# Performance work log

Measured on AMD Instinct MI355X. Metric: run time of the kernel, lower is better.

## Reference

```python
import jax, jax.numpy as jnp
from jax import lax
import numpy as np

N_RES = 2048
N_IN = 64
N_OUT = 32
T = 4096
SPECTRAL_RADIUS = 0.95
NOISE = 0.001


def setup_inputs() -> dict:
    key = jax.random.key(0)
    ks = jax.random.split(key, 8)
    # recurrent weights: uniform(-0.5, 0.5) rescaled to target spectral radius
    w_raw = np.asarray(jax.random.uniform(ks[0], (N_RES, N_RES))) - 0.5
    radius = np.max(np.abs(np.linalg.eigvals(w_raw)))
    w = jnp.asarray((w_raw * (SPECTRAL_RADIUS / radius)).astype(np.float32))
    w_in = jax.random.uniform(ks[1], (N_RES, N_IN), dtype=jnp.float32) * 2.0 - 1.0
    w_feedb = jax.random.uniform(ks[2], (N_RES, N_OUT), dtype=jnp.float32) * 2.0 - 1.0
    # readout (nn.Linear)
    out_w = jax.random.normal(ks[3], (N_OUT, N_RES), dtype=jnp.float32) * 0.02
    out_b = jax.random.normal(ks[4], (N_OUT,), dtype=jnp.float32) * 0.02
    inputs = jax.random.normal(ks[5], (T, N_IN), dtype=jnp.float32)
    outputs = jax.random.normal(ks[6], (T, N_OUT), dtype=jnp.float32)
    # per-step uniform noise (torch.rand equivalent), precomputed for determinism
    noise_u = jax.random.uniform(ks[7], (T, N_RES), dtype=jnp.float32)
    return {"inputs": inputs, "outputs": outputs, "w": w, "w_in": w_in,
            "w_feedb": w_feedb, "out_w": out_w, "out_b": out_b, "noise_u": noise_u}


def reference(inputs, outputs, w, w_in, w_feedb, out_w, out_b, noise_u):
    # Faithful ESN forward with teacher forcing:
    #   state[n] = tanh(w @ state[n-1] + w_in @ inputs[n] + w_feedb @ outputs[n-1])
    #              + noise * (u[n] - 0.5),   n = 1..T-1, state[0] = 0
    # returns (Linear(state[-1]), state[-1])
    def step(state, xs):
        inp, outp_prev, nu = xs
        pre = w @ state + w_in @ inp + w_feedb @ outp_prev
        new_state = jnp.tanh(pre) + NOISE * (nu - 0.5)
        return new_state, None

    state0 = jnp.zeros((w.shape[0],), dtype=inputs.dtype)
    last_state, _ = lax.scan(step, state0, (inputs[1:], outputs[:-1], noise_u[1:]))
    out_activation = out_w @ last_state + out_b
    return out_activation, last_state
```

## Files before the change

kernel.cpp:

```cpp
#include <hip/hip_runtime.h>


#define N_RES   2048
#define N_IN    64
#define N_OUT   32
#define T_STEPS 4096
#define NOISEC  0.001f
#define NBLK    256
#define NTHR    256
#define RPB     8
#define CPT     8

typedef float f32x4 __attribute__((ext_vector_type(4)));

__device__ __forceinline__ float fast_tanh(float x) {
    const float e = __builtin_amdgcn_exp2f(2.8853900818f * x);
    return fmaf(-2.f, __builtin_amdgcn_rcpf(e + 1.f), 1.f);
}

__global__ void esn_init(unsigned long long* __restrict__ slots) {
    const int i = blockIdx.x * blockDim.x + threadIdx.x;
    if (i < 2 * N_RES)
        __hip_atomic_store(slots + i, 0ull, __ATOMIC_RELAXED, __HIP_MEMORY_SCOPE_AGENT);
}

__global__ __launch_bounds__(NTHR, 1)
void esn_run(const float* __restrict__ inputs,
             const float* __restrict__ outputs,
             const float* __restrict__ w,
             const float* __restrict__ w_in,
             const float* __restrict__ w_feedb,
             const float* __restrict__ out_w,
             const float* __restrict__ out_b,
             const float* __restrict__ noise_u,
             float* __restrict__ d_out,
             unsigned long long* __restrict__ slots) {
    const int tid  = threadIdx.x;
    const int blk  = blockIdx.x;
    const int row0 = blk * RPB;
    const int wav  = tid >> 6;
    const int lan  = tid & 63;

    __shared__ float wlds[2 * 8 * NTHR * 4];
    __shared__ float red[2][4][RPB];

    #pragma unroll
    for (int r = 0; r < RPB; ++r)
        #pragma unroll
        for (int cc = 0; cc < 8; ++cc) {
            const float v = w[(size_t)(row0 + r) * N_RES + cc * NTHR + tid];
            wlds[(((r >> 2) * 8 + cc) * NTHR + tid) * 4 + (r & 3)] = v;
        }
    float wex[RPB];
    #pragma unroll
    for (int r = 0; r < RPB; ++r) {
        float v = 0.f;
        if (tid < N_IN)              v = w_in[(row0 + r) * N_IN + tid];
        else if (tid < N_IN + N_OUT) v = w_feedb[(row0 + r) * N_OUT + (tid - N_IN)];
        wex[r] = v;
    }
    __syncthreads();

    for (int t = 1; t < T_STEPS; ++t) {
        f32x4 wv[16];
        #pragma unroll
        for (int rr = 0; rr < 2; ++rr)
            #pragma unroll
            for (int cc = 0; cc < 8; ++cc)
                wv[rr * 8 + cc] = *reinterpret_cast<const f32x4*>(
                    &wlds[((rr * 8 + cc) * NTHR + tid) * 4]);

        float xv = 0.f;
        if (tid < N_IN)              xv = inputs[t * N_IN + tid];
        else if (tid < N_IN + N_OUT) xv = outputs[(t - 1) * N_OUT + (tid - N_IN)];
        float nu = 0.f;
        if (tid < RPB) nu = noise_u[(size_t)t * N_RES + row0 + tid];

        asm volatile("" ::: "memory");

        const unsigned long long* sl = slots + (size_t)((t - 1) & 1) * N_RES + tid;
        const unsigned need = (unsigned)(t - 1);
        unsigned long long vv[CPT];
        #pragma unroll
        for (int i = 0; i < CPT; ++i)
            vv[i] = __hip_atomic_load(sl + i * NTHR, __ATOMIC_RELAXED, __HIP_MEMORY_SCOPE_AGENT);
        for (;;) {
            unsigned mn = 0xffffffffu;
            #pragma unroll
            for (int i = 0; i < CPT; ++i) {
                const unsigned tg = (unsigned)(vv[i] >> 32);
                mn = (tg < mn) ? tg : mn;
            }
            if (mn >= need) break;
            __builtin_amdgcn_s_sleep(1);
            #pragma unroll
            for (int i = 0; i < CPT; ++i)
                if ((unsigned)(vv[i] >> 32) < need)
                    vv[i] = __hip_atomic_load(sl + i * NTHR, __ATOMIC_RELAXED, __HIP_MEMORY_SCOPE_AGENT);
        }

        float acc[RPB];
        #pragma unroll
        for (int r = 0; r < RPB; ++r) acc[r] = 0.f;
        #pragma unroll
        for (int i = 0; i < CPT; ++i) {
            const float sv = __uint_as_float((unsigned)(vv[i] & 0xffffffffu));
            #pragma unroll
            for (int rr = 0; rr < 2; ++rr)
                #pragma unroll
                for (int j = 0; j < 4; ++j)
                    acc[rr * 4 + j] = fmaf(wv[rr * 8 + i][j], sv, acc[rr * 4 + j]);
        }
        #pragma unroll
        for (int r = 0; r < RPB; ++r) acc[r] = fmaf(wex[r], xv, acc[r]);

        {   const bool b = (lan & 1);
            #pragma unroll
            for (int r = 0; r < 4; ++r) {
                const float send = b ? acc[r] : acc[r + 4];
                const float got  = __shfl_xor(send, 1, 64);
                acc[r] = (b ? acc[r + 4] : acc[r]) + got;
            }
        }
        {   const bool b = (lan >> 1) & 1;
            #pragma unroll
            for (int r = 0; r < 2; ++r) {
                const float send = b ? acc[r] : acc[r + 2];
                const float got  = __shfl_xor(send, 2, 64);
                acc[r] = (b ? acc[r + 2] : acc[r]) + got;
            }
        }
        {   const bool b = (lan >> 2) & 1;
            const float send = b ? acc[0] : acc[1];
            const float got  = __shfl_xor(send, 4, 64);
            acc[0] = (b ? acc[1] : acc[0]) + got;
        }
        #pragma unroll
        for (int m = 8; m < 64; m <<= 1) acc[0] += __shfl_xor(acc[0], m, 64);
        if (lan < 8) {
            const int rb = 4 * (lan & 1) + 2 * ((lan >> 1) & 1) + ((lan >> 2) & 1);
            red[t & 1][wav][rb] = acc[0];
        }
        __syncthreads();

        if (tid < RPB) {
            const float tot = red[t & 1][0][tid] + red[t & 1][1][tid]
                            + red[t & 1][2][tid] + red[t & 1][3][tid];
            const float val = fast_tanh(tot) + NOISEC * (nu - 0.5f);
            const unsigned long long pk =
                ((unsigned long long)(unsigned)t << 32) |
                (unsigned long long)__float_as_uint(val);
            __hip_atomic_store(slots + (size_t)(t & 1) * N_RES + row0 + tid, pk,
                               __ATOMIC_RELAXED, __HIP_MEMORY_SCOPE_AGENT);
            if (t == T_STEPS - 1) d_out[32 + row0 + tid] = val;
        }
    }

    if (blk == 0) {
        const unsigned long long* sf = slots + (size_t)((T_STEPS - 1) & 1) * N_RES;
        const int r2 = tid >> 3, j2 = tid & 7;
        const unsigned need = (unsigned)(T_STEPS - 1);
        float acc = 0.f;
        for (int c0 = 0; c0 < N_RES / 8; c0 += 8) {
            const unsigned long long* p = sf + j2 * (N_RES / 8) + c0;
            unsigned long long vv[8];
            #pragma unroll
            for (int i = 0; i < 8; ++i)
                vv[i] = __hip_atomic_load(p + i, __ATOMIC_RELAXED, __HIP_MEMORY_SCOPE_AGENT);
            for (;;) {
                unsigned mn = 0xffffffffu;
                #pragma unroll
                for (int i = 0; i < 8; ++i) {
                    const unsigned tg = (unsigned)(vv[i] >> 32);
                    mn = (tg < mn) ? tg : mn;
                }
                if (mn >= need) break;
                __builtin_amdgcn_s_sleep(1);
                #pragma unroll
                for (int i = 0; i < 8; ++i)
                    if ((unsigned)(vv[i] >> 32) < need)
                        vv[i] = __hip_atomic_load(p + i, __ATOMIC_RELAXED, __HIP_MEMORY_SCOPE_AGENT);
            }
            #pragma unroll
            for (int i = 0; i < 8; ++i) {
                const float sv = __uint_as_float((unsigned)(vv[i] & 0xffffffffu));
                acc = fmaf(out_w[r2 * N_RES + j2 * (N_RES / 8) + c0 + i], sv, acc);
            }
        }
        #pragma unroll
        for (int m = 1; m < 8; m <<= 1) acc += __shfl_xor(acc, m, 64);
        if (j2 == 0) d_out[r2] = acc + out_b[r2];
    }
}

extern "C" void kernel_launch(void* const* d_in, const int* in_sizes, int n_in,
                              void* d_out, int out_size, void* d_ws, size_t ws_size,
                              hipStream_t stream) {
    const float* inputs  = (const float*)d_in[0];
    const float* outputs = (const float*)d_in[1];
    const float* w       = (const float*)d_in[2];
    const float* w_in    = (const float*)d_in[3];
    const float* w_feedb = (const float*)d_in[4];
    const float* out_w   = (const float*)d_in[5];
    const float* out_b   = (const float*)d_in[6];
    const float* noise_u = (const float*)d_in[7];
    unsigned long long* slots = (unsigned long long*)d_ws;

    esn_init<<<(2 * N_RES + NTHR - 1) / NTHR, NTHR, 0, stream>>>(slots);
    esn_run<<<NBLK, NTHR, 0, stream>>>(inputs, outputs, w, w_in, w_feedb,
                                       out_w, out_b, noise_u,
                                       (float*)d_out, slots);
}
```

Measured before the change: 8.087 ms.

## Halve block count with 16 rows per block and consume state slots incrementally

Each block now owns 16 reservoir rows instead of 8, so 128 blocks replace 256 and fewer producers and consumers take part in the per-step global handshake. The spin-wait now accumulates partial dot products as soon as individual state slots arrive, instead of waiting for all of them first, so polling latency overlaps with FMA work. The slot loads are issued before the LDS weight loads. In exchange, each block carries twice the weight registers and FMA work per step, which raises register pressure and lengthens per-step compute on the critical path.

Result: slower. 10.41 ms (+28.8%).

```diff
diff --git a/kernel.cpp b/kernel.cpp
--- a/kernel.cpp
+++ b/kernel.cpp
@@ -6,9 +6,9 @@
 #define N_OUT   32
 #define T_STEPS 4096
 #define NOISEC  0.001f
-#define NBLK    256
+#define NBLK    128
 #define NTHR    256
-#define RPB     8
+#define RPB     16
 #define CPT     8
 
 typedef float f32x4 __attribute__((ext_vector_type(4)));
@@ -41,7 +41,7 @@
     const int wav  = tid >> 6;
     const int lan  = tid & 63;
 
-    __shared__ float wlds[2 * 8 * NTHR * 4];
+    __shared__ float wlds[4 * 8 * NTHR * 4];
     __shared__ float red[2][4][RPB];
 
     #pragma unroll
@@ -62,13 +62,13 @@
     __syncthreads();
 
     for (int t = 1; t < T_STEPS; ++t) {
-        f32x4 wv[16];
-        #pragma unroll
-        for (int rr = 0; rr < 2; ++rr)
-            #pragma unroll
-            for (int cc = 0; cc < 8; ++cc)
-                wv[rr * 8 + cc] = *reinterpret_cast<const f32x4*>(
-                    &wlds[((rr * 8 + cc) * NTHR + tid) * 4]);
+        const unsigned need = (unsigned)(t - 1);
+        const unsigned long long* sl = slots + (size_t)((t - 1) & 1) * N_RES + tid;
+
+        unsigned long long vv[CPT];
+        #pragma unroll
+        for (int i = 0; i < CPT; ++i)
+            vv[i] = __hip_atomic_load(sl + i * NTHR, __ATOMIC_RELAXED, __HIP_MEMORY_SCOPE_AGENT);
 
         float xv = 0.f;
         if (tid < N_IN)              xv = inputs[t * N_IN + tid];
@@ -76,70 +76,80 @@
         float nu = 0.f;
         if (tid < RPB) nu = noise_u[(size_t)t * N_RES + row0 + tid];
 
+        f32x4 wv[32];
+        #pragma unroll
+        for (int rr = 0; rr < 4; ++rr)
+            #pragma unroll
+            for (int cc = 0; cc < 8; ++cc)
+                wv[rr * 8 + cc] = *reinterpret_cast<const f32x4*>(
+                    &wlds[((rr * 8 + cc) * NTHR + tid) * 4]);
+
         asm volatile("" ::: "memory");
 
-        const unsigned long long* sl = slots + (size_t)((t - 1) & 1) * N_RES + tid;
-        const unsigned need = (unsigned)(t - 1);
-        unsigned long long vv[CPT];
-        #pragma unroll
-        for (int i = 0; i < CPT; ++i)
-            vv[i] = __hip_atomic_load(sl + i * NTHR, __ATOMIC_RELAXED, __HIP_MEMORY_SCOPE_AGENT);
+        float acc[RPB];
+        #pragma unroll
+        for (int r = 0; r < RPB; ++r) acc[r] = 0.f;
+        unsigned done = 0;
         for (;;) {
-            unsigned mn = 0xffffffffu;
-            #pragma unroll
-            for (int i = 0; i < CPT; ++i) {
-                const unsigned tg = (unsigned)(vv[i] >> 32);
-                mn = (tg < mn) ? tg : mn;
-            }
-            if (mn >= need) break;
+            unsigned fresh = 0;
+            #pragma unroll
+            for (int i = 0; i < CPT; ++i)
+                if (!((done >> i) & 1) && (unsigned)(vv[i] >> 32) >= need)
+                    fresh |= 1u << i;
+            #pragma unroll
+            for (int i = 0; i < CPT; ++i)
+                if ((fresh >> i) & 1) {
+                    const float sv = __uint_as_float((unsigned)(vv[i] & 0xffffffffu));
+                    #pragma unroll
+                    for (int rr = 0; rr < 4; ++rr)
+                        #pragma unroll
+                        for (int j = 0; j < 4; ++j)
+                            acc[rr * 4 + j] = fmaf(wv[rr * 8 + i][j], sv, acc[rr * 4 + j]);
+                }
+            done |= fresh;
+            if (done == 0xffu) break;
             __builtin_amdgcn_s_sleep(1);
             #pragma unroll
             for (int i = 0; i < CPT; ++i)
-                if ((unsigned)(vv[i] >> 32) < need)
+                if (!((done >> i) & 1))
                     vv[i] = __hip_atomic_load(sl + i * NTHR, __ATOMIC_RELAXED, __HIP_MEMORY_SCOPE_AGENT);
         }
-
-        float acc[RPB];
-        #pragma unroll
-        for (int r = 0; r < RPB; ++r) acc[r] = 0.f;
-        #pragma unroll
-        for (int i = 0; i < CPT; ++i) {
-            const float sv = __uint_as_float((unsigned)(vv[i] & 0xffffffffu));
-            #pragma unroll
-            for (int rr = 0; rr < 2; ++rr)
-                #pragma unroll
-                for (int j = 0; j < 4; ++j)
-                    acc[rr * 4 + j] = fmaf(wv[rr * 8 + i][j], sv, acc[rr * 4 + j]);
-        }
         #pragma unroll
         for (int r = 0; r < RPB; ++r) acc[r] = fmaf(wex[r], xv, acc[r]);
 
         {   const bool b = (lan & 1);
+            #pragma unroll
+            for (int r = 0; r < 8; ++r) {
+                const float send = b ? acc[r] : acc[r + 8];
+                const float got  = __shfl_xor(send, 1, 64);
+                acc[r] = (b ? acc[r + 8] : acc[r]) + got;
+            }
+        }
+        {   const bool b = (lan >> 1) & 1;
             #pragma unroll
             for (int r = 0; r < 4; ++r) {
                 const float send = b ? acc[r] : acc[r + 4];
-                const float got  = __shfl_xor(send, 1, 64);
+                const float got  = __shfl_xor(send, 2, 64);
                 acc[r] = (b ? acc[r + 4] : acc[r]) + got;
             }
         }
-        {   const bool b = (lan >> 1) & 1;
+        {   const bool b = (lan >> 2) & 1;
             #pragma unroll
             for (int r = 0; r < 2; ++r) {
                 const float send = b ? acc[r] : acc[r + 2];
-                const float got  = __shfl_xor(send, 2, 64);
+                const float got  = __shfl_xor(send, 4, 64);
                 acc[r] = (b ? acc[r + 2] : acc[r]) + got;
             }
         }
-        {   const bool b = (lan >> 2) & 1;
-            const float send = b ? acc[0] : acc[1];
-            const float got  = __shfl_xor(send, 4, 64);
-            acc[0] = (b ? acc[1] : acc[0]) + got;
-        }
-        #pragma unroll
-        for (int m = 8; m < 64; m <<= 1) acc[0] += __shfl_xor(acc[0], m, 64);
+        #pragma unroll
+        for (int m = 8; m < 64; m <<= 1) {
+            acc[0] += __shfl_xor(acc[0], m, 64);
+            acc[1] += __shfl_xor(acc[1], m, 64);
+        }
         if (lan < 8) {
-            const int rb = 4 * (lan & 1) + 2 * ((lan >> 1) & 1) + ((lan >> 2) & 1);
-            red[t & 1][wav][rb] = acc[0];
+            const int rb = 8 * (lan & 1) + 4 * ((lan >> 1) & 1) + 2 * ((lan >> 2) & 1);
+            red[t & 1][wav][rb]     = acc[0];
+            red[t & 1][wav][rb + 1] = acc[1];
         }
         __syncthreads();
 
```

## Use contiguous per-thread state columns and issue slot loads before LDS weight reads

Applied to the files above, without the earlier changes.

Each thread now owns 8 contiguous state columns (tid*8+i), so its polling loads hit adjacent 64-bit slots. Each row of W is re-laid out in LDS to match this mapping. The state slot loads are issued before the LDS weight reads and the x/noise loads, so global latency overlaps them. The spin loop skips the sleep on its first retry and reloads all 8 slots unconditionally instead of only the stale ones. This trades fewer cache lines per thread and lower wake-up latency for more polling traffic and a less coalesced pattern across lanes.

New measurement: 17.78 ms, median of 2. 2.2x slower.

```diff
diff --git a/kernel.cpp b/kernel.cpp
--- a/kernel.cpp
+++ b/kernel.cpp
@@ -47,9 +47,9 @@
     #pragma unroll
     for (int r = 0; r < RPB; ++r)
         #pragma unroll
-        for (int cc = 0; cc < 8; ++cc) {
-            const float v = w[(size_t)(row0 + r) * N_RES + cc * NTHR + tid];
-            wlds[(((r >> 2) * 8 + cc) * NTHR + tid) * 4 + (r & 3)] = v;
+        for (int i = 0; i < CPT; ++i) {
+            const float v = w[(size_t)(row0 + r) * N_RES + 8 * tid + i];
+            wlds[(((r >> 2) * 8 + i) * NTHR + tid) * 4 + (r & 3)] = v;
         }
     float wex[RPB];
     #pragma unroll
@@ -62,13 +62,14 @@
     __syncthreads();
 
     for (int t = 1; t < T_STEPS; ++t) {
-        f32x4 wv[16];
-        #pragma unroll
-        for (int rr = 0; rr < 2; ++rr)
-            #pragma unroll
-            for (int cc = 0; cc < 8; ++cc)
-                wv[rr * 8 + cc] = *reinterpret_cast<const f32x4*>(
-                    &wlds[((rr * 8 + cc) * NTHR + tid) * 4]);
+        const unsigned need = (unsigned)(t - 1);
+        const unsigned long long* sl =
+            slots + (size_t)((t - 1) & 1) * N_RES + tid * CPT;
+
+        unsigned long long vv[CPT];
+        #pragma unroll
+        for (int i = 0; i < CPT; ++i)
+            vv[i] = __hip_atomic_load(sl + i, __ATOMIC_RELAXED, __HIP_MEMORY_SCOPE_AGENT);
 
         float xv = 0.f;
         if (tid < N_IN)              xv = inputs[t * N_IN + tid];
@@ -76,14 +77,17 @@
         float nu = 0.f;
         if (tid < RPB) nu = noise_u[(size_t)t * N_RES + row0 + tid];
 
+        f32x4 wv[16];
+        #pragma unroll
+        for (int rr = 0; rr < 2; ++rr)
+            #pragma unroll
+            for (int i = 0; i < CPT; ++i)
+                wv[rr * 8 + i] = *reinterpret_cast<const f32x4*>(
+                    &wlds[((rr * 8 + i) * NTHR + tid) * 4]);
+
         asm volatile("" ::: "memory");
 
-        const unsigned long long* sl = slots + (size_t)((t - 1) & 1) * N_RES + tid;
-        const unsigned need = (unsigned)(t - 1);
-        unsigned long long vv[CPT];
-        #pragma unroll
-        for (int i = 0; i < CPT; ++i)
-            vv[i] = __hip_atomic_load(sl + i * NTHR, __ATOMIC_RELAXED, __HIP_MEMORY_SCOPE_AGENT);
+        int tries = 0;
         for (;;) {
             unsigned mn = 0xffffffffu;
             #pragma unroll
@@ -92,11 +96,10 @@
                 mn = (tg < mn) ? tg : mn;
             }
             if (mn >= need) break;
-            __builtin_amdgcn_s_sleep(1);
+            if (++tries > 1) __builtin_amdgcn_s_sleep(1);
             #pragma unroll
             for (int i = 0; i < CPT; ++i)
-                if ((unsigned)(vv[i] >> 32) < need)
-                    vv[i] = __hip_atomic_load(sl + i * NTHR, __ATOMIC_RELAXED, __HIP_MEMORY_SCOPE_AGENT);
+                vv[i] = __hip_atomic_load(sl + i, __ATOMIC_RELAXED, __HIP_MEMORY_SCOPE_AGENT);
         }
 
         float acc[RPB];
@@ -114,26 +117,26 @@
         #pragma unroll
         for (int r = 0; r < RPB; ++r) acc[r] = fmaf(wex[r], xv, acc[r]);
 
-        {   const bool b = (lan & 1);
+        {   const bool s = (lan & 1);
             #pragma unroll
             for (int r = 0; r < 4; ++r) {
-                const float send = b ? acc[r] : acc[r + 4];
+                const float send = s ? acc[r] : acc[r + 4];
                 const float got  = __shfl_xor(send, 1, 64);
-                acc[r] = (b ? acc[r + 4] : acc[r]) + got;
-            }
-        }
-        {   const bool b = (lan >> 1) & 1;
+                acc[r] = (s ? acc[r + 4] : acc[r]) + got;
+            }
+        }
+        {   const bool s = (lan >> 1) & 1;
             #pragma unroll
             for (int r = 0; r < 2; ++r) {
-                const float send = b ? acc[r] : acc[r + 2];
+                const float send = s ? acc[r] : acc[r + 2];
                 const float got  = __shfl_xor(send, 2, 64);
-                acc[r] = (b ? acc[r + 2] : acc[r]) + got;
-            }
-        }
-        {   const bool b = (lan >> 2) & 1;
-            const float send = b ? acc[0] : acc[1];
+                acc[r] = (s ? acc[r + 2] : acc[r]) + got;
+            }
+        }
+        {   const bool s = (lan >> 2) & 1;
+            const float send = s ? acc[0] : acc[1];
             const float got  = __shfl_xor(send, 4, 64);
-            acc[0] = (b ? acc[1] : acc[0]) + got;
+            acc[0] = (s ? acc[1] : acc[0]) + got;
         }
         #pragma unroll
         for (int m = 8; m < 64; m <<= 1) acc[0] += __shfl_xor(acc[0], m, 64);
@@ -183,8 +186,8 @@
             }
             #pragma unroll
             for (int i = 0; i < 8; ++i) {
-                const float sv = __uint_as_float((unsigned)(vv[i] & 0xffffffffu));
-                acc = fmaf(out_w[r2 * N_RES + j2 * (N_RES / 8) + c0 + i], sv, acc);
+                const float s = __uint_as_float((unsigned)(vv[i] & 0xffffffffu));
+                acc = fmaf(out_w[r2 * N_RES + j2 * (N_RES / 8) + c0 + i], s, acc);
             }
         }
         #pragma unroll
```
